# Kernel optimization log

Hardware: AMD Instinct MI355X
Metric: run time of the kernel (lower is better)

The kernel has to match this reference:

```python
import jax, jax.numpy as jnp
import numpy as np

N_NODES = 50000
N_EDGES = 800000
IN_DIM = 128
EDGE_DIM = 128
OUT_DIM = 128
N_AGG = 4          # mean, max, min, std
N_SCALE = 3        # identity, amplification, attenuation
AVG_D_LOG = float(np.log(17.0))  # log(avg_degree + 1), PNA avg_d['log']
EPS = 1e-5


def setup_inputs() -> dict:
    key = jax.random.key(0)
    ks = jax.random.split(key, 10)
    pre_in = 2 * IN_DIM + EDGE_DIM                      # pretrans input dim
    post_in = (N_AGG * N_SCALE + 1) * IN_DIM            # posttrans input dim
    return {
        "node_feat": jax.random.normal(ks[0], (N_NODES, IN_DIM), jnp.float32),
        "edge_feat": jax.random.normal(ks[1], (N_EDGES, EDGE_DIM), jnp.float32),
        "w_pre": jax.random.normal(ks[2], (pre_in, IN_DIM), jnp.float32) * (1.0 / np.sqrt(pre_in)),
        "b_pre": jnp.zeros((IN_DIM,), jnp.float32),
        "w_post1": jax.random.normal(ks[3], (post_in, OUT_DIM), jnp.float32) * (1.0 / np.sqrt(post_in)),
        "b_post1": jnp.zeros((OUT_DIM,), jnp.float32),
        "w_post2": jax.random.normal(ks[4], (OUT_DIM, OUT_DIM), jnp.float32) * (1.0 / np.sqrt(OUT_DIM)),
        "b_post2": jnp.zeros((OUT_DIM,), jnp.float32),
        "src": jax.random.randint(ks[5], (N_EDGES,), 0, N_NODES, jnp.int32),
        "dst": jax.random.randint(ks[6], (N_EDGES,), 0, N_NODES, jnp.int32),
    }


def reference(node_feat, edge_feat, w_pre, b_pre, w_post1, b_post1,
              w_post2, b_post2, src, dst):
    n = node_feat.shape[0]
    # --- pretrans over edges: MLP(cat[src_h, dst_h, edge_feat]) -> message ---
    z = jnp.concatenate([node_feat[src], node_feat[dst], edge_feat], axis=-1)  # [E, 2d+de]
    msg = jax.nn.relu(z @ w_pre + b_pre)                                       # [E, d]

    # --- multi-aggregator scatter-reduce per destination node ---
    ones = jnp.ones((msg.shape[0],), msg.dtype)
    deg = jax.ops.segment_sum(ones, dst, num_segments=n)                       # [N]
    d_safe = jnp.maximum(deg, 1.0)[:, None]
    has_nb = (deg > 0)[:, None]

    s1 = jax.ops.segment_sum(msg, dst, num_segments=n)
    s2 = jax.ops.segment_sum(msg * msg, dst, num_segments=n)
    a_mean = s1 / d_safe
    a_var = jax.nn.relu(s2 / d_safe - a_mean * a_mean)
    a_std = jnp.sqrt(a_var + EPS)
    a_max = jnp.where(has_nb, jax.ops.segment_max(msg, dst, num_segments=n), 0.0)
    a_min = jnp.where(has_nb, jax.ops.segment_min(msg, dst, num_segments=n), 0.0)
    agg = jnp.concatenate([a_mean, a_max, a_min, a_std], axis=-1)              # [N, 4d]

    # --- degree scalers: identity, amplification, attenuation ---
    logd = jnp.log(deg + 1.0)[:, None]
    amp = agg * (logd / AVG_D_LOG)
    att = agg * (AVG_D_LOG / jnp.maximum(logd, EPS))
    h = jnp.concatenate([node_feat, agg, amp, att], axis=-1)                   # [N, 13d]

    # --- posttrans MLP + residual ---
    h1 = jax.nn.relu(h @ w_post1 + b_post1)
    out = h1 @ w_post2 + b_post2 + node_feat                                   # residual (in_dim == out_dim)
    return out
```

## Files before the change

kernel.cpp:

```cpp
#include <hip/hip_runtime.h>
#include <math.h>

#define N_NODES 50000
#define N_EDGES 800000
#define D 128
#define AVG_D_LOG 2.833213344056216f
#define EPS 1e-5f

typedef __attribute__((ext_vector_type(8))) short bf16x8;
typedef __attribute__((ext_vector_type(4))) float f32x4;

__device__ __forceinline__ unsigned short f2bf(float x) {
    unsigned u = __float_as_uint(x);
    u += 0x7fffu + ((u >> 16) & 1u);
    return (unsigned short)(u >> 16);
}
__device__ __forceinline__ unsigned pk2bf(float a, float b) {
    return (unsigned)f2bf(a) | ((unsigned)f2bf(b) << 16);
}
__device__ __forceinline__ float bf2f(unsigned short u) {
    return __uint_as_float(((unsigned)u) << 16);
}

__global__ void k_init(int* hist, float* s1, float* s2, float* mx, float* mn) {
    size_t stride = (size_t)gridDim.x * blockDim.x;
    size_t i0 = (size_t)blockIdx.x * blockDim.x + threadIdx.x;
    const size_t ND4 = (size_t)N_NODES * D / 4;
    float4 z4 = {0.f, 0.f, 0.f, 0.f};
    int4 inf4 = {0x7f800000, 0x7f800000, 0x7f800000, 0x7f800000};
    for (size_t t = i0; t < ND4; t += stride) {
        ((float4*)s1)[t] = z4; ((float4*)s2)[t] = z4; ((float4*)mx)[t] = z4;
        ((int4*)mn)[t] = inf4;
    }
    for (size_t t = i0; t < N_NODES; t += stride) hist[t] = 0;
}

__global__ void k_init_h(int* hist) {
    int i = blockIdx.x * blockDim.x + threadIdx.x;
    if (i < N_NODES) hist[i] = 0;
}

__global__ void k_hist(const int* __restrict__ dst, int* hist) {
    int e = blockIdx.x * blockDim.x + threadIdx.x;
    if (e < N_EDGES) atomicAdd(&hist[dst[e]], 1);
}

__global__ void k_scan(const int* __restrict__ hist, int* cursor) {
    __shared__ int part[256];
    __shared__ int base_s[256];
    int t = threadIdx.x;
    const int chunk = (N_NODES + 255) / 256;
    int lo = t * chunk;
    int hi = lo + chunk; if (hi > N_NODES) hi = N_NODES;
    int s = 0;
    for (int i = lo; i < hi; ++i) s += hist[i];
    part[t] = s;
    __syncthreads();
    if (t == 0) {
        int run = 0;
        for (int i = 0; i < 256; ++i) { base_s[i] = run; run += part[i]; }
    }
    __syncthreads();
    int run = base_s[t];
    for (int i = lo; i < hi; ++i) { cursor[i] = run; run += hist[i]; }
}

__global__ void k_scatter(const int* __restrict__ dst, int* cursor, int* perm) {
    int e = blockIdx.x * blockDim.x + threadIdx.x;
    if (e < N_EDGES) {
        int pos = atomicAdd(&cursor[dst[e]], 1);
        perm[pos] = e;
    }
}

__global__ void k_prepT(const float* __restrict__ w, unsigned short* __restrict__ wT, int K) {
    int idx = blockIdx.x * blockDim.x + threadIdx.x;
    if (idx >= K * D) return;
    int k = idx >> 7, c = idx & 127;
    wT[(size_t)c * K + k] = f2bf(w[idx]);
}

#define ZROW(NC, e) ((NC) < 2 ? nf + (size_t)sidx[e] * D : \
                     (NC) < 4 ? nf + (size_t)didx[e] * D : \
                                ef + (size_t)pidx[e] * D)
#define PF(NC) do { \
    { int g = t;       int c = g >> 3, j = g & 7;  pw0 = *(const uint4*)(wpT + (size_t)c * 384 + (NC) * 64 + j * 8); } \
    { int g = t + 256; int c = g >> 3, j = g & 7;  pw1 = *(const uint4*)(wpT + (size_t)c * 384 + (NC) * 64 + j * 8); } \
    { int g = t + 512; int c = g >> 3, j = g & 7;  pw2 = *(const uint4*)(wpT + (size_t)c * 384 + (NC) * 64 + j * 8); } \
    { int g = t + 768; int c = g >> 3, j = g & 7;  pw3 = *(const uint4*)(wpT + (size_t)c * 384 + (NC) * 64 + j * 8); } \
    { int g = t;       int e = g >> 4, q = g & 15; pz0 = *(const float4*)(ZROW(NC, e) + (((NC) & 1) * 64) + q * 4); } \
    { int g = t + 256; int e = g >> 4, q = g & 15; pz1 = *(const float4*)(ZROW(NC, e) + (((NC) & 1) * 64) + q * 4); } \
    { int g = t + 512; int e = g >> 4, q = g & 15; pz2 = *(const float4*)(ZROW(NC, e) + (((NC) & 1) * 64) + q * 4); } \
    { int g = t + 768; int e = g >> 4, q = g & 15; pz3 = *(const float4*)(ZROW(NC, e) + (((NC) & 1) * 64) + q * 4); } \
} while (0)
#define WR() do { \
    { int g = t;       int c = g >> 3, j = g & 7;  *(uint4*)(smem + c * 128 + ((j * 16) ^ ((c & 7) << 4))) = pw0; } \
    { int g = t + 256; int c = g >> 3, j = g & 7;  *(uint4*)(smem + c * 128 + ((j * 16) ^ ((c & 7) << 4))) = pw1; } \
    { int g = t + 512; int c = g >> 3, j = g & 7;  *(uint4*)(smem + c * 128 + ((j * 16) ^ ((c & 7) << 4))) = pw2; } \
    { int g = t + 768; int c = g >> 3, j = g & 7;  *(uint4*)(smem + c * 128 + ((j * 16) ^ ((c & 7) << 4))) = pw3; } \
    { int g = t;       int e = g >> 4, q = g & 15; uint2 hv = { pk2bf(pz0.x, pz0.y), pk2bf(pz0.z, pz0.w) }; \
      *(uint2*)(smem + 16384 + e * 128 + ((q * 8) ^ ((e & 7) << 4))) = hv; } \
    { int g = t + 256; int e = g >> 4, q = g & 15; uint2 hv = { pk2bf(pz1.x, pz1.y), pk2bf(pz1.z, pz1.w) }; \
      *(uint2*)(smem + 16384 + e * 128 + ((q * 8) ^ ((e & 7) << 4))) = hv; } \
    { int g = t + 512; int e = g >> 4, q = g & 15; uint2 hv = { pk2bf(pz2.x, pz2.y), pk2bf(pz2.z, pz2.w) }; \
      *(uint2*)(smem + 16384 + e * 128 + ((q * 8) ^ ((e & 7) << 4))) = hv; } \
    { int g = t + 768; int e = g >> 4, q = g & 15; uint2 hv = { pk2bf(pz3.x, pz3.y), pk2bf(pz3.z, pz3.w) }; \
      *(uint2*)(smem + 16384 + e * 128 + ((q * 8) ^ ((e & 7) << 4))) = hv; } \
} while (0)
#define MM() do { \
    _Pragma("unroll") \
    for (int ks = 0; ks < 2; ++ks) { \
        bf16x8 afr[2], bfr[4]; \
        int kb = ks * 64 + lg * 16; \
        _Pragma("unroll") \
        for (int cf = 0; cf < 2; ++cf) { \
            int c = w * 32 + cf * 16 + lr; \
            afr[cf] = *(const bf16x8*)(smem + c * 128 + (kb ^ ((c & 7) << 4))); \
        } \
        _Pragma("unroll") \
        for (int eb = 0; eb < 4; ++eb) { \
            int e = eb * 16 + lr; \
            bfr[eb] = *(const bf16x8*)(smem + 16384 + e * 128 + (kb ^ ((e & 7) << 4))); \
        } \
        _Pragma("unroll") \
        for (int cf = 0; cf < 2; ++cf) \
            _Pragma("unroll") \
            for (int eb = 0; eb < 4; ++eb) \
                acc[cf][eb] = __builtin_amdgcn_mfma_f32_16x16x32_bf16( \
                    afr[cf], bfr[eb], acc[cf][eb], 0, 0, 0); \
    } \
} while (0)

__global__ __launch_bounds__(256) void k_pretrans_g(
    const float* __restrict__ nf, const float* __restrict__ ef,
    const unsigned short* __restrict__ wpT, const float* __restrict__ bp,
    const int* __restrict__ src, const int* __restrict__ dst,
    const int* __restrict__ perm,
    unsigned short* __restrict__ msgG)
{
    __shared__ __align__(16) char smem[24576];
    __shared__ int pidx[64], sidx[64], didx[64];
    __shared__ float sb[128];

    int t = threadIdx.x;
    int e0 = blockIdx.x * 64;
    if (t < 64) {
        int pe = perm[e0 + t];
        pidx[t] = pe; sidx[t] = src[pe]; didx[t] = dst[pe];
    }
    if (t < 128) sb[t] = bp[t];
    __syncthreads();

    int w  = t >> 6;
    int l  = t & 63;
    int lr = l & 15;
    int lg = l >> 4;

    f32x4 acc[2][4];
    #pragma unroll
    for (int i = 0; i < 2; ++i)
        #pragma unroll
        for (int j = 0; j < 4; ++j) acc[i][j] = (f32x4){0.f, 0.f, 0.f, 0.f};

    uint4  pw0, pw1, pw2, pw3;
    float4 pz0, pz1, pz2, pz3;

    PF(0);
    WR(); PF(1); __syncthreads(); MM(); __syncthreads();
    WR(); PF(2); __syncthreads(); MM(); __syncthreads();
    WR(); PF(3); __syncthreads(); MM(); __syncthreads();
    WR(); PF(4); __syncthreads(); MM(); __syncthreads();
    WR(); PF(5); __syncthreads(); MM(); __syncthreads();
    WR();        __syncthreads(); MM(); __syncthreads();

    #pragma unroll
    for (int cf = 0; cf < 2; ++cf)
        #pragma unroll
        for (int eb = 0; eb < 4; ++eb) {
            int e  = eb * 16 + lr;
            int c0 = w * 32 + cf * 16 + lg * 4;
            float v0 = fmaxf(acc[cf][eb][0] + sb[c0 + 0], 0.f);
            float v1 = fmaxf(acc[cf][eb][1] + sb[c0 + 1], 0.f);
            float v2 = fmaxf(acc[cf][eb][2] + sb[c0 + 2], 0.f);
            float v3 = fmaxf(acc[cf][eb][3] + sb[c0 + 3], 0.f);
            uint2 mv = { pk2bf(v0, v1), pk2bf(v2, v3) };
            *(uint2*)(smem + e * 256 + ((c0 * 2) ^ ((e & 7) << 4))) = mv;
        }
    __syncthreads();
    #pragma unroll
    for (int p = 0; p < 4; ++p) {
        int e = (t >> 4) + p * 16;
        int q = t & 15;
        uint4 v = *(const uint4*)(smem + e * 256 + q * 16);
        int qq = q ^ (e & 7);
        *(uint4*)(msgG + (size_t)(e0 + e) * D + qq * 8) = v;
    }
}

__global__ __launch_bounds__(256) void k_agg(
    const unsigned short* __restrict__ msgG,
    const int* __restrict__ cursor, const int* __restrict__ hist,
    float* __restrict__ s1, float* __restrict__ s2,
    float* __restrict__ mx, float* __restrict__ mn, float* __restrict__ scal)
{
    int t = threadIdx.x;
    int n = blockIdx.x * 4 + (t >> 6);
    int tl = t & 63;
    int deg = hist[n];
    int re  = cursor[n];
    int rs  = re - deg;

    float sum0 = 0.f, sum1 = 0.f, sq0 = 0.f, sq1 = 0.f;
    float mx0 = -3.402823e38f, mx1 = -3.402823e38f;
    float mn0 =  3.402823e38f, mn1 =  3.402823e38f;
    const uint* mg = (const uint*)msgG;
    for (int e = 0; e < deg; ++e) {
        uint v = mg[(size_t)(rs + e) * 64 + tl];
        float a = bf2f((unsigned short)(v & 0xffff));
        float b = bf2f((unsigned short)(v >> 16));
        sum0 += a; sum1 += b; sq0 += a * a; sq1 += b * b;
        mx0 = fmaxf(mx0, a); mx1 = fmaxf(mx1, b);
        mn0 = fminf(mn0, a); mn1 = fminf(mn1, b);
    }
    float dg = (float)deg;
    float ds = fmaxf(dg, 1.f);
    bool nb = deg > 0;
    float m0 = sum0 / ds, m1 = sum1 / ds;
    float sd0 = sqrtf(fmaxf(sq0 / ds - m0 * m0, 0.f) + EPS);
    float sd1 = sqrtf(fmaxf(sq1 / ds - m1 * m1, 0.f) + EPS);
    size_t base = (size_t)n * D + tl * 2;
    *(float2*)&s1[base] = (float2){m0, m1};
    *(float2*)&s2[base] = (float2){sd0, sd1};
    *(float2*)&mx[base] = (float2){nb ? mx0 : 0.f, nb ? mx1 : 0.f};
    *(float2*)&mn[base] = (float2){nb ? mn0 : 0.f, nb ? mn1 : 0.f};
    if (tl == 0) {
        float logd = logf(dg + 1.f);
        scal[2 * n]     = logd / AVG_D_LOG;
        scal[2 * n + 1] = AVG_D_LOG / fmaxf(logd, EPS);
    }
}

__global__ __launch_bounds__(256) void k_pretrans(
    const float* __restrict__ nf, const float* __restrict__ ef,
    const unsigned short* __restrict__ wpT, const float* __restrict__ bp,
    const int* __restrict__ src, const int* __restrict__ dst,
    const int* __restrict__ perm,
    float* s1, float* s2, float* mx, float* mn)
{
    __shared__ __align__(16) char smem[24576];
    __shared__ int pidx[64], sidx[64], didx[64];
    __shared__ int seg_start[65], seg_dst[64];
    __shared__ int nseg_s;
    __shared__ float sb[128];

    int t = threadIdx.x;
    int e0 = blockIdx.x * 64;
    if (t < 64) {
        int pe = perm[e0 + t];
        pidx[t] = pe; sidx[t] = src[pe]; didx[t] = dst[pe];
    }
    if (t < 128) sb[t] = bp[t];
    __syncthreads();

    int w  = t >> 6;
    int l  = t & 63;
    int lr = l & 15;
    int lg = l >> 4;

    f32x4 acc[2][4];
    #pragma unroll
    for (int i = 0; i < 2; ++i)
        #pragma unroll
        for (int j = 0; j < 4; ++j) acc[i][j] = (f32x4){0.f, 0.f, 0.f, 0.f};

    uint4  pw0, pw1, pw2, pw3;
    float4 pz0, pz1, pz2, pz3;

    PF(0);
    WR(); PF(1); __syncthreads(); MM(); __syncthreads();
    WR(); PF(2); __syncthreads(); MM(); __syncthreads();
    WR(); PF(3); __syncthreads(); MM(); __syncthreads();
    WR(); PF(4); __syncthreads(); MM(); __syncthreads();
    WR(); PF(5); __syncthreads(); MM(); __syncthreads();
    WR();        __syncthreads(); MM(); __syncthreads();

    #pragma unroll
    for (int cf = 0; cf < 2; ++cf)
        #pragma unroll
        for (int eb = 0; eb < 4; ++eb) {
            int e  = eb * 16 + lr;
            int c0 = w * 32 + cf * 16 + lg * 4;
            float v0 = fmaxf(acc[cf][eb][0] + sb[c0 + 0], 0.f);
            float v1 = fmaxf(acc[cf][eb][1] + sb[c0 + 1], 0.f);
            float v2 = fmaxf(acc[cf][eb][2] + sb[c0 + 2], 0.f);
            float v3 = fmaxf(acc[cf][eb][3] + sb[c0 + 3], 0.f);
            uint2 mv = { pk2bf(v0, v1), pk2bf(v2, v3) };
            *(uint2*)(smem + e * 256 + ((c0 * 2) ^ ((e & 7) << 4))) = mv;
        }
    if (t == 0) {
        int ns = 0;
        for (int e = 0; e < 64; ++e) {
            if (e == 0 || didx[e] != didx[e - 1]) { seg_dst[ns] = didx[e]; seg_start[ns] = e; ++ns; }
        }
        seg_start[ns] = 64; nseg_s = ns;
    }
    __syncthreads();
    int nseg = nseg_s;
    for (int idx = t; idx < nseg * D; idx += 256) {
        int sg = idx >> 7, c = idx & 127;
        int eb2 = seg_start[sg], ee = seg_start[sg + 1];
        float s = 0.f, q = 0.f, vmax = 0.f, vmin = __int_as_float(0x7f800000);
        for (int e = eb2; e < ee; ++e) {
            float v = bf2f(*(const unsigned short*)(smem + e * 256 + ((c * 2) ^ ((e & 7) << 4))));
            s += v; q += v * v;
            vmax = fmaxf(vmax, v); vmin = fminf(vmin, v);
        }
        size_t base = (size_t)seg_dst[sg] * D + c;
        atomicAdd(&s1[base], s);
        atomicAdd(&s2[base], q);
        atomicMax((int*)&mx[base], __float_as_int(vmax));
        atomicMin((int*)&mn[base], __float_as_int(vmin));
    }
}

#undef ZROW
#undef PF
#undef WR
#undef MM

__global__ void k_finalize(float* s1, float* s2, float* mx, float* mn,
                           const int* __restrict__ hist, float* scal) {
    size_t idx = (size_t)blockIdx.x * blockDim.x + threadIdx.x;
    if (idx >= (size_t)N_NODES * D) return;
    int n = (int)(idx >> 7);
    int c = (int)(idx & 127);
    float dg = (float)hist[n];
    float ds = fmaxf(dg, 1.f);
    float m  = s1[idx] / ds;
    float var = fmaxf(s2[idx] / ds - m * m, 0.f);
    float sd  = sqrtf(var + EPS);
    bool nb = dg > 0.f;
    s1[idx] = m;
    mx[idx] = nb ? mx[idx] : 0.f;
    mn[idx] = nb ? mn[idx] : 0.f;
    s2[idx] = sd;
    if (c == 0) {
        float logd = logf(dg + 1.f);
        scal[2 * n]     = logd / AVG_D_LOG;
        scal[2 * n + 1] = AVG_D_LOG / fmaxf(logd, EPS);
    }
}

__global__ __launch_bounds__(256, 3) void k_post1(
    const float* __restrict__ nf,
    const float* __restrict__ amean, const float* __restrict__ amax,
    const float* __restrict__ amin,  const float* __restrict__ astd,
    const float* __restrict__ scal,
    const unsigned short* __restrict__ w1T, const float* __restrict__ b1,
    unsigned short* __restrict__ h1bf)
{
    __shared__ __align__(16) char smem[49152];
    __shared__ float samp[64], satt[64], sb[128];

    int t = threadIdx.x;
    int n0 = blockIdx.x * 64;
    if (t < 64) {
        int n = n0 + t;
        samp[t] = (n < N_NODES) ? scal[2 * n] : 0.f;
        satt[t] = (n < N_NODES) ? scal[2 * n + 1] : 0.f;
    }
    if (t < 128) sb[t] = b1[t];
    __syncthreads();

    int w  = t >> 6, l = t & 63, lr = l & 15, lg = l >> 4;
    f32x4 acc[2][4];
    #pragma unroll
    for (int i = 0; i < 2; ++i)
        #pragma unroll
        for (int j = 0; j < 4; ++j) acc[i][j] = (f32x4){0.f, 0.f, 0.f, 0.f};

    for (int chunk = 0; chunk < 13; ++chunk) {
        #pragma unroll
        for (int p = 0; p < 8; ++p) {
            int g = t + 256 * p;
            int c = g >> 4, j = g & 15;
            uint4 wv = *(const uint4*)(w1T + (size_t)c * 1664 + chunk * 128 + j * 8);
            *(uint4*)(smem + c * 256 + ((j * 16) ^ ((c & 7) << 4))) = wv;
        }
        const float* base;
        int r;
        if (chunk == 0) { base = nf; r = 0; }
        else {
            int b = (chunk - 1) & 3;
            r = (chunk - 1) >> 2;
            base = (b == 0) ? amean : (b == 1) ? amax : (b == 2) ? amin : astd;
        }
        #pragma unroll
        for (int p = 0; p < 8; ++p) {
            int g = t + 256 * p;
            int e = g >> 5, q = g & 31;
            int n = n0 + e;
            float4 fv = {0.f, 0.f, 0.f, 0.f};
            if (n < N_NODES) {
                fv = *(const float4*)(base + (size_t)n * D + q * 4);
                if (r == 1) { float sc = samp[e]; fv.x *= sc; fv.y *= sc; fv.z *= sc; fv.w *= sc; }
                else if (r == 2) { float sc = satt[e]; fv.x *= sc; fv.y *= sc; fv.z *= sc; fv.w *= sc; }
            }
            uint2 hv = { pk2bf(fv.x, fv.y), pk2bf(fv.z, fv.w) };
            *(uint2*)(smem + 32768 + e * 256 + ((q * 8) ^ ((e & 7) << 4))) = hv;
        }
        __syncthreads();
        #pragma unroll
        for (int ks = 0; ks < 4; ++ks) {
            bf16x8 afr[2], bfr[4];
            int kb = ks * 64 + lg * 16;
            #pragma unroll
            for (int cf = 0; cf < 2; ++cf) {
                int c = w * 32 + cf * 16 + lr;
                afr[cf] = *(const bf16x8*)(smem + c * 256 + (kb ^ ((c & 7) << 4)));
            }
            #pragma unroll
            for (int eb = 0; eb < 4; ++eb) {
                int e = eb * 16 + lr;
                bfr[eb] = *(const bf16x8*)(smem + 32768 + e * 256 + (kb ^ ((e & 7) << 4)));
            }
            #pragma unroll
            for (int cf = 0; cf < 2; ++cf)
                #pragma unroll
                for (int eb = 0; eb < 4; ++eb)
                    acc[cf][eb] = __builtin_amdgcn_mfma_f32_16x16x32_bf16(
                        afr[cf], bfr[eb], acc[cf][eb], 0, 0, 0);
        }
        __syncthreads();
    }

    #pragma unroll
    for (int cf = 0; cf < 2; ++cf)
        #pragma unroll
        for (int eb = 0; eb < 4; ++eb) {
            int n = n0 + eb * 16 + lr;
            if (n < N_NODES) {
                int c0 = w * 32 + cf * 16 + lg * 4;
                float v0 = fmaxf(acc[cf][eb][0] + sb[c0 + 0], 0.f);
                float v1 = fmaxf(acc[cf][eb][1] + sb[c0 + 1], 0.f);
                float v2 = fmaxf(acc[cf][eb][2] + sb[c0 + 2], 0.f);
                float v3 = fmaxf(acc[cf][eb][3] + sb[c0 + 3], 0.f);
                uint2 hv = { pk2bf(v0, v1), pk2bf(v2, v3) };
                *(uint2*)(h1bf + (size_t)n * D + c0) = hv;
            }
        }
}

__global__ __launch_bounds__(256, 3) void k_post2(
    const unsigned short* __restrict__ h1bf, const unsigned short* __restrict__ w2T,
    const float* __restrict__ b2, const float* __restrict__ nf,
    float* __restrict__ out)
{
    __shared__ __align__(16) char smem[49152];
    __shared__ float sb[128];

    int t = threadIdx.x;
    int n0 = blockIdx.x * 64;
    if (t < 128) sb[t] = b2[t];

    int w  = t >> 6, l = t & 63, lr = l & 15, lg = l >> 4;
    f32x4 acc[2][4];
    #pragma unroll
    for (int i = 0; i < 2; ++i)
        #pragma unroll
        for (int j = 0; j < 4; ++j) acc[i][j] = (f32x4){0.f, 0.f, 0.f, 0.f};

    #pragma unroll
    for (int p = 0; p < 8; ++p) {
        int g = t + 256 * p;
        int c = g >> 4, j = g & 15;
        uint4 wv = *(const uint4*)(w2T + (size_t)c * 128 + j * 8);
        *(uint4*)(smem + c * 256 + ((j * 16) ^ ((c & 7) << 4))) = wv;
    }
    #pragma unroll
    for (int p = 0; p < 4; ++p) {
        int g = t + 256 * p;
        int e = g >> 4, j = g & 15;
        int n = n0 + e;
        uint4 hv = {0u, 0u, 0u, 0u};
        if (n < N_NODES) hv = *(const uint4*)(h1bf + (size_t)n * D + j * 8);
        *(uint4*)(smem + 32768 + e * 256 + ((j * 16) ^ ((e & 7) << 4))) = hv;
    }
    __syncthreads();
    #pragma unroll
    for (int ks = 0; ks < 4; ++ks) {
        bf16x8 afr[2], bfr[4];
        int kb = ks * 64 + lg * 16;
        #pragma unroll
        for (int cf = 0; cf < 2; ++cf) {
            int c = w * 32 + cf * 16 + lr;
            afr[cf] = *(const bf16x8*)(smem + c * 256 + (kb ^ ((c & 7) << 4)));
        }
        #pragma unroll
        for (int eb = 0; eb < 4; ++eb) {
            int e = eb * 16 + lr;
            bfr[eb] = *(const bf16x8*)(smem + 32768 + e * 256 + (kb ^ ((e & 7) << 4)));
        }
        #pragma unroll
        for (int cf = 0; cf < 2; ++cf)
            #pragma unroll
            for (int eb = 0; eb < 4; ++eb)
                acc[cf][eb] = __builtin_amdgcn_mfma_f32_16x16x32_bf16(
                    afr[cf], bfr[eb], acc[cf][eb], 0, 0, 0);
    }

    #pragma unroll
    for (int cf = 0; cf < 2; ++cf)
        #pragma unroll
        for (int eb = 0; eb < 4; ++eb) {
            int n = n0 + eb * 16 + lr;
            if (n < N_NODES) {
                int c0 = w * 32 + cf * 16 + lg * 4;
                float4 rv = *(const float4*)(nf + (size_t)n * D + c0);
                float4 ov = { acc[cf][eb][0] + sb[c0 + 0] + rv.x,
                              acc[cf][eb][1] + sb[c0 + 1] + rv.y,
                              acc[cf][eb][2] + sb[c0 + 2] + rv.z,
                              acc[cf][eb][3] + sb[c0 + 3] + rv.w };
                *(float4*)(out + (size_t)n * D + c0) = ov;
            }
        }
}

extern "C" void kernel_launch(void* const* d_in, const int* in_sizes, int n_in,
                              void* d_out, int out_size, void* d_ws, size_t ws_size,
                              hipStream_t stream) {
    const float* nf = (const float*)d_in[0];
    const float* ef = (const float*)d_in[1];
    const float* wp = (const float*)d_in[2];
    const float* bp = (const float*)d_in[3];
    const float* w1 = (const float*)d_in[4];
    const float* b1 = (const float*)d_in[5];
    const float* w2 = (const float*)d_in[6];
    const float* b2 = (const float*)d_in[7];
    const int* src  = (const int*)d_in[8];
    const int* dst  = (const int*)d_in[9];
    float* out = (float*)d_out;

    const size_t ND = (size_t)N_NODES * D;
    char* wsb = (char*)d_ws;
    int*   hist   = (int*)wsb;
    int*   cursor = hist + 50048;
    int*   perm   = cursor + 50048;
    unsigned short* wpT = (unsigned short*)(perm + N_EDGES);
    unsigned short* w1T = wpT + 49152;
    unsigned short* w2T = w1T + 212992;
    unsigned short* msgG = w2T + 16384;
    const size_t MSG_SH = (size_t)N_EDGES * D;
    float* s1     = (float*)(msgG + MSG_SH);
    float* s2     = s1 + ND;
    float* mx     = s2 + ND;
    float* mn     = mx + ND;
    float* scal   = mn + ND;
    unsigned short* h1bf = (unsigned short*)(scal + 100096);
    size_t need_csr = (size_t)((char*)(h1bf + ND) - wsb);

    bool use_csr = ws_size >= need_csr;
    if (!use_csr) {
        s1   = (float*)(w2T + 16384);
        s2   = s1 + ND;
        mx   = s2 + ND;
        mn   = mx + ND;
        scal = mn + ND;
        h1bf = (unsigned short*)(scal + 100096);
    }

    if (use_csr) {
        hipLaunchKernelGGL(k_init_h, dim3((N_NODES + 255) / 256), dim3(256), 0, stream, hist);
    } else {
        hipLaunchKernelGGL(k_init, dim3(2048), dim3(256), 0, stream, hist, s1, s2, mx, mn);
    }
    hipLaunchKernelGGL(k_hist, dim3((N_EDGES + 255) / 256), dim3(256), 0, stream, dst, hist);
    hipLaunchKernelGGL(k_scan, dim3(1), dim3(256), 0, stream, hist, cursor);
    hipLaunchKernelGGL(k_scatter, dim3((N_EDGES + 255) / 256), dim3(256), 0, stream, dst, cursor, perm);
    hipLaunchKernelGGL(k_prepT, dim3(192), dim3(256), 0, stream, wp, wpT, 384);
    hipLaunchKernelGGL(k_prepT, dim3(832), dim3(256), 0, stream, w1, w1T, 1664);
    hipLaunchKernelGGL(k_prepT, dim3(64),  dim3(256), 0, stream, w2, w2T, 128);
    if (use_csr) {
        hipLaunchKernelGGL(k_pretrans_g, dim3(N_EDGES / 64), dim3(256), 0, stream,
                           nf, ef, wpT, bp, src, dst, perm, msgG);
        hipLaunchKernelGGL(k_agg, dim3(N_NODES / 4), dim3(256), 0, stream,
                           msgG, cursor, hist, s1, s2, mx, mn, scal);
    } else {
        hipLaunchKernelGGL(k_pretrans, dim3(N_EDGES / 64), dim3(256), 0, stream,
                           nf, ef, wpT, bp, src, dst, perm, s1, s2, mx, mn);
        hipLaunchKernelGGL(k_finalize, dim3((unsigned)((ND + 255) / 256)), dim3(256), 0, stream,
                           s1, s2, mx, mn, hist, scal);
    }
    hipLaunchKernelGGL(k_post1, dim3((N_NODES + 63) / 64), dim3(256), 0, stream,
                       nf, s1, mx, mn, s2, scal, w1T, b1, h1bf);
    hipLaunchKernelGGL(k_post2, dim3((N_NODES + 63) / 64), dim3(256), 0, stream,
                       h1bf, w2T, b2, nf, out);
}
```

Before: 611.9 us.

## Double-buffer pretrans LDS tiles and store aggregates as bf16

The gather-GEMM pretrans kernel now keeps two LDS buffers, so the next K-chunk is written while MFMA runs on the previous one, which removes one barrier per stage. This doubles its shared memory to 48 KB, which may lower occupancy. Separately, the aggregator outputs (mean, max, min, std) are stored as bf16 instead of fp32. This halves the traffic written by k_agg and read by k_post1, but the amp/att scaling is now applied to bf16-rounded values.

```diff
diff --git a/kernel.cpp b/kernel.cpp
--- a/kernel.cpp
+++ b/kernel.cpp
@@ -83,31 +83,31 @@
 #define ZROW(NC, e) ((NC) < 2 ? nf + (size_t)sidx[e] * D : \
                      (NC) < 4 ? nf + (size_t)didx[e] * D : \
                                 ef + (size_t)pidx[e] * D)
-#define PF(NC) do { \
-    { int g = t;       int c = g >> 3, j = g & 7;  pw0 = *(const uint4*)(wpT + (size_t)c * 384 + (NC) * 64 + j * 8); } \
-    { int g = t + 256; int c = g >> 3, j = g & 7;  pw1 = *(const uint4*)(wpT + (size_t)c * 384 + (NC) * 64 + j * 8); } \
-    { int g = t + 512; int c = g >> 3, j = g & 7;  pw2 = *(const uint4*)(wpT + (size_t)c * 384 + (NC) * 64 + j * 8); } \
-    { int g = t + 768; int c = g >> 3, j = g & 7;  pw3 = *(const uint4*)(wpT + (size_t)c * 384 + (NC) * 64 + j * 8); } \
-    { int g = t;       int e = g >> 4, q = g & 15; pz0 = *(const float4*)(ZROW(NC, e) + (((NC) & 1) * 64) + q * 4); } \
-    { int g = t + 256; int e = g >> 4, q = g & 15; pz1 = *(const float4*)(ZROW(NC, e) + (((NC) & 1) * 64) + q * 4); } \
-    { int g = t + 512; int e = g >> 4, q = g & 15; pz2 = *(const float4*)(ZROW(NC, e) + (((NC) & 1) * 64) + q * 4); } \
-    { int g = t + 768; int e = g >> 4, q = g & 15; pz3 = *(const float4*)(ZROW(NC, e) + (((NC) & 1) * 64) + q * 4); } \
+#define PFN(NC, PW0, PW1, PW2, PW3, PZ0, PZ1, PZ2, PZ3) do { \
+    { int g = t;       int c = g >> 3, j = g & 7;  PW0 = *(const uint4*)(wpT + (size_t)c * 384 + (NC) * 64 + j * 8); } \
+    { int g = t + 256; int c = g >> 3, j = g & 7;  PW1 = *(const uint4*)(wpT + (size_t)c * 384 + (NC) * 64 + j * 8); } \
+    { int g = t + 512; int c = g >> 3, j = g & 7;  PW2 = *(const uint4*)(wpT + (size_t)c * 384 + (NC) * 64 + j * 8); } \
+    { int g = t + 768; int c = g >> 3, j = g & 7;  PW3 = *(const uint4*)(wpT + (size_t)c * 384 + (NC) * 64 + j * 8); } \
+    { int g = t;       int e = g >> 4, q = g & 15; PZ0 = *(const float4*)(ZROW(NC, e) + (((NC) & 1) * 64) + q * 4); } \
+    { int g = t + 256; int e = g >> 4, q = g & 15; PZ1 = *(const float4*)(ZROW(NC, e) + (((NC) & 1) * 64) + q * 4); } \
+    { int g = t + 512; int e = g >> 4, q = g & 15; PZ2 = *(const float4*)(ZROW(NC, e) + (((NC) & 1) * 64) + q * 4); } \
+    { int g = t + 768; int e = g >> 4, q = g & 15; PZ3 = *(const float4*)(ZROW(NC, e) + (((NC) & 1) * 64) + q * 4); } \
 } while (0)
-#define WR() do { \
-    { int g = t;       int c = g >> 3, j = g & 7;  *(uint4*)(smem + c * 128 + ((j * 16) ^ ((c & 7) << 4))) = pw0; } \
-    { int g = t + 256; int c = g >> 3, j = g & 7;  *(uint4*)(smem + c * 128 + ((j * 16) ^ ((c & 7) << 4))) = pw1; } \
-    { int g = t + 512; int c = g >> 3, j = g & 7;  *(uint4*)(smem + c * 128 + ((j * 16) ^ ((c & 7) << 4))) = pw2; } \
-    { int g = t + 768; int c = g >> 3, j = g & 7;  *(uint4*)(smem + c * 128 + ((j * 16) ^ ((c & 7) << 4))) = pw3; } \
-    { int g = t;       int e = g >> 4, q = g & 15; uint2 hv = { pk2bf(pz0.x, pz0.y), pk2bf(pz0.z, pz0.w) }; \
-      *(uint2*)(smem + 16384 + e * 128 + ((q * 8) ^ ((e & 7) << 4))) = hv; } \
-    { int g = t + 256; int e = g >> 4, q = g & 15; uint2 hv = { pk2bf(pz1.x, pz1.y), pk2bf(pz1.z, pz1.w) }; \
-      *(uint2*)(smem + 16384 + e * 128 + ((q * 8) ^ ((e & 7) << 4))) = hv; } \
-    { int g = t + 512; int e = g >> 4, q = g & 15; uint2 hv = { pk2bf(pz2.x, pz2.y), pk2bf(pz2.z, pz2.w) }; \
-      *(uint2*)(smem + 16384 + e * 128 + ((q * 8) ^ ((e & 7) << 4))) = hv; } \
-    { int g = t + 768; int e = g >> 4, q = g & 15; uint2 hv = { pk2bf(pz3.x, pz3.y), pk2bf(pz3.z, pz3.w) }; \
-      *(uint2*)(smem + 16384 + e * 128 + ((q * 8) ^ ((e & 7) << 4))) = hv; } \
+#define WRN(OFF, PW0, PW1, PW2, PW3, PZ0, PZ1, PZ2, PZ3) do { \
+    { int g = t;       int c = g >> 3, j = g & 7;  *(uint4*)(smem + (OFF) + c * 128 + ((j * 16) ^ ((c & 7) << 4))) = PW0; } \
+    { int g = t + 256; int c = g >> 3, j = g & 7;  *(uint4*)(smem + (OFF) + c * 128 + ((j * 16) ^ ((c & 7) << 4))) = PW1; } \
+    { int g = t + 512; int c = g >> 3, j = g & 7;  *(uint4*)(smem + (OFF) + c * 128 + ((j * 16) ^ ((c & 7) << 4))) = PW2; } \
+    { int g = t + 768; int c = g >> 3, j = g & 7;  *(uint4*)(smem + (OFF) + c * 128 + ((j * 16) ^ ((c & 7) << 4))) = PW3; } \
+    { int g = t;       int e = g >> 4, q = g & 15; uint2 hv = { pk2bf(PZ0.x, PZ0.y), pk2bf(PZ0.z, PZ0.w) }; \
+      *(uint2*)(smem + (OFF) + 16384 + e * 128 + ((q * 8) ^ ((e & 7) << 4))) = hv; } \
+    { int g = t + 256; int e = g >> 4, q = g & 15; uint2 hv = { pk2bf(PZ1.x, PZ1.y), pk2bf(PZ1.z, PZ1.w) }; \
+      *(uint2*)(smem + (OFF) + 16384 + e * 128 + ((q * 8) ^ ((e & 7) << 4))) = hv; } \
+    { int g = t + 512; int e = g >> 4, q = g & 15; uint2 hv = { pk2bf(PZ2.x, PZ2.y), pk2bf(PZ2.z, PZ2.w) }; \
+      *(uint2*)(smem + (OFF) + 16384 + e * 128 + ((q * 8) ^ ((e & 7) << 4))) = hv; } \
+    { int g = t + 768; int e = g >> 4, q = g & 15; uint2 hv = { pk2bf(PZ3.x, PZ3.y), pk2bf(PZ3.z, PZ3.w) }; \
+      *(uint2*)(smem + (OFF) + 16384 + e * 128 + ((q * 8) ^ ((e & 7) << 4))) = hv; } \
 } while (0)
-#define MM() do { \
+#define MMO(OFF) do { \
     _Pragma("unroll") \
     for (int ks = 0; ks < 2; ++ks) { \
         bf16x8 afr[2], bfr[4]; \
@@ -115,12 +115,12 @@
         _Pragma("unroll") \
         for (int cf = 0; cf < 2; ++cf) { \
             int c = w * 32 + cf * 16 + lr; \
-            afr[cf] = *(const bf16x8*)(smem + c * 128 + (kb ^ ((c & 7) << 4))); \
+            afr[cf] = *(const bf16x8*)(smem + (OFF) + c * 128 + (kb ^ ((c & 7) << 4))); \
         } \
         _Pragma("unroll") \
         for (int eb = 0; eb < 4; ++eb) { \
             int e = eb * 16 + lr; \
-            bfr[eb] = *(const bf16x8*)(smem + 16384 + e * 128 + (kb ^ ((e & 7) << 4))); \
+            bfr[eb] = *(const bf16x8*)(smem + (OFF) + 16384 + e * 128 + (kb ^ ((e & 7) << 4))); \
         } \
         _Pragma("unroll") \
         for (int cf = 0; cf < 2; ++cf) \
@@ -138,7 +138,7 @@
     const int* __restrict__ perm,
     unsigned short* __restrict__ msgG)
 {
-    __shared__ __align__(16) char smem[24576];
+    __shared__ __align__(16) char smem[49152];
     __shared__ int pidx[64], sidx[64], didx[64];
     __shared__ float sb[128];
 
@@ -162,16 +162,33 @@
         #pragma unroll
         for (int j = 0; j < 4; ++j) acc[i][j] = (f32x4){0.f, 0.f, 0.f, 0.f};
 
-    uint4  pw0, pw1, pw2, pw3;
-    float4 pz0, pz1, pz2, pz3;
-
-    PF(0);
-    WR(); PF(1); __syncthreads(); MM(); __syncthreads();
-    WR(); PF(2); __syncthreads(); MM(); __syncthreads();
-    WR(); PF(3); __syncthreads(); MM(); __syncthreads();
-    WR(); PF(4); __syncthreads(); MM(); __syncthreads();
-    WR(); PF(5); __syncthreads(); MM(); __syncthreads();
-    WR();        __syncthreads(); MM(); __syncthreads();
+    uint4  pwA0, pwA1, pwA2, pwA3, pwB0, pwB1, pwB2, pwB3;
+    float4 pzA0, pzA1, pzA2, pzA3, pzB0, pzB1, pzB2, pzB3;
+
+    PFN(0, pwA0, pwA1, pwA2, pwA3, pzA0, pzA1, pzA2, pzA3);
+    WRN(0, pwA0, pwA1, pwA2, pwA3, pzA0, pzA1, pzA2, pzA3);
+    PFN(1, pwB0, pwB1, pwB2, pwB3, pzB0, pzB1, pzB2, pzB3);
+    __syncthreads();
+    WRN(24576, pwB0, pwB1, pwB2, pwB3, pzB0, pzB1, pzB2, pzB3);
+    PFN(2, pwA0, pwA1, pwA2, pwA3, pzA0, pzA1, pzA2, pzA3);
+    MMO(0);
+    __syncthreads();
+    WRN(0, pwA0, pwA1, pwA2, pwA3, pzA0, pzA1, pzA2, pzA3);
+    PFN(3, pwB0, pwB1, pwB2, pwB3, pzB0, pzB1, pzB2, pzB3);
+    MMO(24576);
+    __syncthreads();
+    WRN(24576, pwB0, pwB1, pwB2, pwB3, pzB0, pzB1, pzB2, pzB3);
+    PFN(4, pwA0, pwA1, pwA2, pwA3, pzA0, pzA1, pzA2, pzA3);
+    MMO(0);
+    __syncthreads();
+    WRN(0, pwA0, pwA1, pwA2, pwA3, pzA0, pzA1, pzA2, pzA3);
+    PFN(5, pwB0, pwB1, pwB2, pwB3, pzB0, pzB1, pzB2, pzB3);
+    MMO(24576);
+    __syncthreads();
+    WRN(24576, pwB0, pwB1, pwB2, pwB3, pzB0, pzB1, pzB2, pzB3);
+    MMO(0);
+    __syncthreads();
+    MMO(24576);
 
     #pragma unroll
     for (int cf = 0; cf < 2; ++cf)
@@ -200,8 +217,9 @@
 __global__ __launch_bounds__(256) void k_agg(
     const unsigned short* __restrict__ msgG,
     const int* __restrict__ cursor, const int* __restrict__ hist,
-    float* __restrict__ s1, float* __restrict__ s2,
-    float* __restrict__ mx, float* __restrict__ mn, float* __restrict__ scal)
+    unsigned short* __restrict__ agm, unsigned short* __restrict__ ags,
+    unsigned short* __restrict__ agx, unsigned short* __restrict__ agn,
+    float* __restrict__ scal)
 {
     int t = threadIdx.x;
     int n = blockIdx.x * 4 + (t >> 6);
@@ -228,11 +246,11 @@
     float m0 = sum0 / ds, m1 = sum1 / ds;
     float sd0 = sqrtf(fmaxf(sq0 / ds - m0 * m0, 0.f) + EPS);
     float sd1 = sqrtf(fmaxf(sq1 / ds - m1 * m1, 0.f) + EPS);
-    size_t base = (size_t)n * D + tl * 2;
-    *(float2*)&s1[base] = (float2){m0, m1};
-    *(float2*)&s2[base] = (float2){sd0, sd1};
-    *(float2*)&mx[base] = (float2){nb ? mx0 : 0.f, nb ? mx1 : 0.f};
-    *(float2*)&mn[base] = (float2){nb ? mn0 : 0.f, nb ? mn1 : 0.f};
+    size_t ub = (size_t)n * 64 + tl;
+    ((uint*)agm)[ub] = pk2bf(m0, m1);
+    ((uint*)ags)[ub] = pk2bf(sd0, sd1);
+    ((uint*)agx)[ub] = pk2bf(nb ? mx0 : 0.f, nb ? mx1 : 0.f);
+    ((uint*)agn)[ub] = pk2bf(nb ? mn0 : 0.f, nb ? mn1 : 0.f);
     if (tl == 0) {
         float logd = logf(dg + 1.f);
         scal[2 * n]     = logd / AVG_D_LOG;
@@ -276,13 +294,13 @@
     uint4  pw0, pw1, pw2, pw3;
     float4 pz0, pz1, pz2, pz3;
 
-    PF(0);
-    WR(); PF(1); __syncthreads(); MM(); __syncthreads();
-    WR(); PF(2); __syncthreads(); MM(); __syncthreads();
-    WR(); PF(3); __syncthreads(); MM(); __syncthreads();
-    WR(); PF(4); __syncthreads(); MM(); __syncthreads();
-    WR(); PF(5); __syncthreads(); MM(); __syncthreads();
-    WR();        __syncthreads(); MM(); __syncthreads();
+    PFN(0, pw0, pw1, pw2, pw3, pz0, pz1, pz2, pz3);
+    WRN(0, pw0, pw1, pw2, pw3, pz0, pz1, pz2, pz3); PFN(1, pw0, pw1, pw2, pw3, pz0, pz1, pz2, pz3); __syncthreads(); MMO(0); __syncthreads();
+    WRN(0, pw0, pw1, pw2, pw3, pz0, pz1, pz2, pz3); PFN(2, pw0, pw1, pw2, pw3, pz0, pz1, pz2, pz3); __syncthreads(); MMO(0); __syncthreads();
+    WRN(0, pw0, pw1, pw2, pw3, pz0, pz1, pz2, pz3); PFN(3, pw0, pw1, pw2, pw3, pz0, pz1, pz2, pz3); __syncthreads(); MMO(0); __syncthreads();
+    WRN(0, pw0, pw1, pw2, pw3, pz0, pz1, pz2, pz3); PFN(4, pw0, pw1, pw2, pw3, pz0, pz1, pz2, pz3); __syncthreads(); MMO(0); __syncthreads();
+    WRN(0, pw0, pw1, pw2, pw3, pz0, pz1, pz2, pz3); PFN(5, pw0, pw1, pw2, pw3, pz0, pz1, pz2, pz3); __syncthreads(); MMO(0); __syncthreads();
+    WRN(0, pw0, pw1, pw2, pw3, pz0, pz1, pz2, pz3);                                                 __syncthreads(); MMO(0); __syncthreads();
 
     #pragma unroll
     for (int cf = 0; cf < 2; ++cf)
@@ -324,12 +342,14 @@
 }
 
 #undef ZROW
-#undef PF
-#undef WR
-#undef MM
-
-__global__ void k_finalize(float* s1, float* s2, float* mx, float* mn,
-                           const int* __restrict__ hist, float* scal) {
+#undef PFN
+#undef WRN
+#undef MMO
+
+__global__ void k_finalize(const float* s1, const float* s2, const float* mx, const float* mn,
+                           const int* __restrict__ hist,
+                           unsigned short* agm, unsigned short* ags,
+                           unsigned short* agx, unsigned short* agn, float* scal) {
     size_t idx = (size_t)blockIdx.x * blockDim.x + threadIdx.x;
     if (idx >= (size_t)N_NODES * D) return;
     int n = (int)(idx >> 7);
@@ -340,10 +360,10 @@
     float var = fmaxf(s2[idx] / ds - m * m, 0.f);
     float sd  = sqrtf(var + EPS);
     bool nb = dg > 0.f;
-    s1[idx] = m;
-    mx[idx] = nb ? mx[idx] : 0.f;
-    mn[idx] = nb ? mn[idx] : 0.f;
-    s2[idx] = sd;
+    agm[idx] = f2bf(m);
+    agx[idx] = f2bf(nb ? mx[idx] : 0.f);
+    agn[idx] = f2bf(nb ? mn[idx] : 0.f);
+    ags[idx] = f2bf(sd);
     if (c == 0) {
         float logd = logf(dg + 1.f);
         scal[2 * n]     = logd / AVG_D_LOG;
@@ -353,8 +373,8 @@
 
 __global__ __launch_bounds__(256, 3) void k_post1(
     const float* __restrict__ nf,
-    const float* __restrict__ amean, const float* __restrict__ amax,
-    const float* __restrict__ amin,  const float* __restrict__ astd,
+    const unsigned short* __restrict__ agm, const unsigned short* __restrict__ agx,
+    const unsigned short* __restrict__ agn, const unsigned short* __restrict__ ags,
     const float* __restrict__ scal,
     const unsigned short* __restrict__ w1T, const float* __restrict__ b1,
     unsigned short* __restrict__ h1bf)
@@ -387,27 +407,41 @@
             uint4 wv = *(const uint4*)(w1T + (size_t)c * 1664 + chunk * 128 + j * 8);
             *(uint4*)(smem + c * 256 + ((j * 16) ^ ((c & 7) << 4))) = wv;
         }
-        const float* base;
-        int r;
-        if (chunk == 0) { base = nf; r = 0; }
-        else {
+        if (chunk == 0) {
+            #pragma unroll
+            for (int p = 0; p < 8; ++p) {
+                int g = t + 256 * p;
+                int e = g >> 5, q = g & 31;
+                int n = n0 + e;
+                float4 fv = {0.f, 0.f, 0.f, 0.f};
+                if (n < N_NODES) fv = *(const float4*)(nf + (size_t)n * D + q * 4);
+                uint2 hv = { pk2bf(fv.x, fv.y), pk2bf(fv.z, fv.w) };
+                *(uint2*)(smem + 32768 + e * 256 + ((q * 8) ^ ((e & 7) << 4))) = hv;
+            }
+        } else {
             int b = (chunk - 1) & 3;
-            r = (chunk - 1) >> 2;
-            base = (b == 0) ? amean : (b == 1) ? amax : (b == 2) ? amin : astd;
-        }
-        #pragma unroll
-        for (int p = 0; p < 8; ++p) {
-            int g = t + 256 * p;
-            int e = g >> 5, q = g & 31;
-            int n = n0 + e;
-            float4 fv = {0.f, 0.f, 0.f, 0.f};
-            if (n < N_NODES) {
-                fv = *(const float4*)(base + (size_t)n * D + q * 4);
-                if (r == 1) { float sc = samp[e]; fv.x *= sc; fv.y *= sc; fv.z *= sc; fv.w *= sc; }
-                else if (r == 2) { float sc = satt[e]; fv.x *= sc; fv.y *= sc; fv.z *= sc; fv.w *= sc; }
+            int r = (chunk - 1) >> 2;
+            const unsigned short* basb = (b == 0) ? agm : (b == 1) ? agx : (b == 2) ? agn : ags;
+            #pragma unroll
+            for (int p = 0; p < 8; ++p) {
+                int g = t + 256 * p;
+                int e = g >> 5, q = g & 31;
+                int n = n0 + e;
+                uint2 hv = {0u, 0u};
+                if (n < N_NODES) {
+                    uint2 v = *(const uint2*)(basb + (size_t)n * D + q * 4);
+                    if (r == 0) hv = v;
+                    else {
+                        float sc = (r == 1) ? samp[e] : satt[e];
+                        float a0 = bf2f((unsigned short)(v.x & 0xffff)) * sc;
+                        float a1 = bf2f((unsigned short)(v.x >> 16)) * sc;
+                        float a2 = bf2f((unsigned short)(v.y & 0xffff)) * sc;
+                        float a3 = bf2f((unsigned short)(v.y >> 16)) * sc;
+                        hv.x = pk2bf(a0, a1); hv.y = pk2bf(a2, a3);
+                    }
+                }
+                *(uint2*)(smem + 32768 + e * 256 + ((q * 8) ^ ((e & 7) << 4))) = hv;
             }
-            uint2 hv = { pk2bf(fv.x, fv.y), pk2bf(fv.z, fv.w) };
-            *(uint2*)(smem + 32768 + e * 256 + ((q * 8) ^ ((e & 7) << 4))) = hv;
         }
         __syncthreads();
         #pragma unroll
@@ -542,6 +576,7 @@
     float* out = (float*)d_out;
 
     const size_t ND = (size_t)N_NODES * D;
+    const size_t MSG_SH = (size_t)N_EDGES * D;
     char* wsb = (char*)d_ws;
     int*   hist   = (int*)wsb;
     int*   cursor = hist + 50048;
@@ -549,23 +584,29 @@
     unsigned short* wpT = (unsigned short*)(perm + N_EDGES);
     unsigned short* w1T = wpT + 49152;
     unsigned short* w2T = w1T + 212992;
-    unsigned short* msgG = w2T + 16384;
-    const size_t MSG_SH = (size_t)N_EDGES * D;
-    float* s1     = (float*)(msgG + MSG_SH);
-    float* s2     = s1 + ND;
-    float* mx     = s2 + ND;
-    float* mn     = mx + ND;
-    float* scal   = mn + ND;
+    unsigned short* tail = w2T + 16384;
+
+    unsigned short* msgG = tail;
+    unsigned short* agm  = msgG + MSG_SH;
+    unsigned short* agx  = agm + ND;
+    unsigned short* agn  = agx + ND;
+    unsigned short* ags  = agn + ND;
+    float* scal          = (float*)(ags + ND);
     unsigned short* h1bf = (unsigned short*)(scal + 100096);
     size_t need_csr = (size_t)((char*)(h1bf + ND) - wsb);
 
+    float *s1 = nullptr, *s2 = nullptr, *mx = nullptr, *mn = nullptr;
     bool use_csr = ws_size >= need_csr;
     if (!use_csr) {
-        s1   = (float*)(w2T + 16384);
+        s1   = (float*)tail;
         s2   = s1 + ND;
         mx   = s2 + ND;
         mn   = mx + ND;
-        scal = mn + ND;
+        agm  = (unsigned short*)(mn + ND);
+        agx  = agm + ND;
+        agn  = agx + ND;
+        ags  = agn + ND;
+        scal = (float*)(ags + ND);
         h1bf = (unsigned short*)(scal + 100096);
     }
 
@@ -584,15 +625,15 @@
         hipLaunchKernelGGL(k_pretrans_g, dim3(N_EDGES / 64), dim3(256), 0, stream,
                            nf, ef, wpT, bp, src, dst, perm, msgG);
         hipLaunchKernelGGL(k_agg, dim3(N_NODES / 4), dim3(256), 0, stream,
-                           msgG, cursor, hist, s1, s2, mx, mn, scal);
+                           msgG, cursor, hist, agm, ags, agx, agn, scal);
     } else {
         hipLaunchKernelGGL(k_pretrans, dim3(N_EDGES / 64), dim3(256), 0, stream,
                            nf, ef, wpT, bp, src, dst, perm, s1, s2, mx, mn);
         hipLaunchKernelGGL(k_finalize, dim3((unsigned)((ND + 255) / 256)), dim3(256), 0, stream,
-                           s1, s2, mx, mn, hist, scal);
+                           s1, s2, mx, mn, hist, agm, ags, agx, agn, scal);
     }
     hipLaunchKernelGGL(k_post1, dim3((N_NODES + 63) / 64), dim3(256), 0, stream,
-                       nf, s1, mx, mn, s2, scal, w1T, b1, h1bf);
+                       nf, agm, agx, agn, ags, scal, w1T, b1, h1bf);
     hipLaunchKernelGGL(k_post2, dim3((N_NODES + 63) / 64), dim3(256), 0, stream,
                        h1bf, w2T, b2, nf, out);
 }
```

After: 643.0 us. 5.1% more time.
